# Optimization experiments

Measured on AMD Instinct MI355X. Metric: run time of the kernel, lower is better.

The kernel has to match this reference:

```python
import jax, jax.numpy as jnp
import numpy as np

K = 20
BN_EPS = 1e-5
NEG_SLOPE = 0.2


def knn_idx(x, k):
    # x: [B, C, N]; returns indices of k nearest neighbors per point: [B, N, k]
    sq = jnp.sum(x * x, axis=1)                      # [B, N]
    inner = jnp.einsum('bcn,bcm->bnm', x, x)         # [B, N, N]
    dist = sq[:, :, None] + sq[:, None, :] - 2.0 * inner  # squared distances
    _, idx = jax.lax.top_k(-dist, k)                 # smallest distances
    return idx


def get_graph_feature(x, k):
    # x: [B, C, N] -> [B, 2C, N, k]
    idx = knn_idx(x, k)                               # [B, N, k]
    gather = lambda xb, ib: xb[:, ib]                 # [C,N] x [N,k] -> [C,N,k]
    feature = jax.vmap(gather)(x, idx)                # [B, C, N, k]
    xk = jnp.broadcast_to(x[:, :, :, None], feature.shape)
    return jnp.concatenate([feature - xk, xk], axis=1)  # [B, 2C, N, k]


def setup_inputs() -> dict:
    key = jax.random.key(0)
    k1, k2 = jax.random.split(key)
    B, C, N = 8, 64, 4096
    x = jax.random.normal(k1, (B, C, N), dtype=jnp.float32)
    W = jax.random.normal(k2, (64, 2 * C), dtype=jnp.float32) * (1.0 / np.sqrt(2 * C))
    gamma = jnp.ones((64,), dtype=jnp.float32)
    beta = jnp.zeros((64,), dtype=jnp.float32)
    return {"x": x, "W": W, "gamma": gamma, "beta": beta}


def reference(x, W, gamma, beta):
    g = get_graph_feature(x, K)                       # [B, 2C, N, k]
    y = jnp.einsum('oc,bcnk->bonk', W, g)             # 1x1 conv, no bias
    # BatchNorm2d (training-mode batch statistics) over (B, N, k) per channel
    mean = jnp.mean(y, axis=(0, 2, 3), keepdims=True)
    var = jnp.var(y, axis=(0, 2, 3), keepdims=True)
    y = (y - mean) * jax.lax.rsqrt(var + BN_EPS)
    y = y * gamma[None, :, None, None] + beta[None, :, None, None]
    # LeakyReLU(0.2)
    y = jnp.where(y >= 0, y, NEG_SLOPE * y)
    # max over neighbors
    return jnp.max(y, axis=-1)                        # [B, out, N]
```

## Files before the change

### kernel.cpp

```cpp
#include <hip/hip_runtime.h>
#include <hip/hip_bf16.h>
#include <float.h>

#define BATCH 8
#define CDIM 64
#define NPTS 4096
#define KNN 20
#define KSEL 32
#define BUFCAP 128
#define BN_EPS 1e-5f
#define NEG_SLOPE 0.2f

typedef __attribute__((ext_vector_type(8))) short short8;
typedef __attribute__((ext_vector_type(4))) float float4v;
typedef unsigned short ushort;
typedef unsigned int uint;
typedef unsigned long long ull;

__device__ __forceinline__ ushort f2bf(float f) {
    uint u = __float_as_uint(f);
    u += 0x7FFF + ((u >> 16) & 1);
    return (ushort)(u >> 16);
}
__device__ __forceinline__ int mbcnt64(ull m) {
    int c = __builtin_amdgcn_mbcnt_lo((uint)m, 0);
    return __builtin_amdgcn_mbcnt_hi((uint)(m >> 32), c);
}

__device__ __forceinline__ uint select33_truncate(uint* __restrict__ buf,
                                                  int& cnt, int lane) {
    uint e0 = 0xFFFFFFFFu, e1 = 0xFFFFFFFFu;
    if (lane < cnt) e0 = buf[lane];
    if (64 + lane < cnt) e1 = buf[64 + lane];
    uint p = 0;
    for (int bit = 31; bit >= 0; --bit) {
        uint t = p | (1u << bit);
        ull mA = __ballot(e0 < t);
        ull mB = __ballot(e1 < t);
        if (__popcll(mA) + __popcll(mB) < 33) p = t;
    }
    ull mA = __ballot(e0 < p);
    ull mB = __ballot(e1 < p);
    int pA = __popcll(mA);
    int r0 = mbcnt64(mA);
    int r1 = pA + mbcnt64(mB);
    if (e0 < p) buf[r0] = e0;
    if (e1 < p) buf[r1] = e1;
    cnt = pA + __popcll(mB);
    return p;
}

__device__ __forceinline__ void scan_append(float dwv, float base, int idx,
                                            uint& tau, int& cnt,
                                            uint* __restrict__ buf, int lane) {
    float dval = fmaxf(fmaf(-2.f, dwv, base), 0.f);
    uint key = (__float_as_uint(dval) & 0xFFFFF000u) | (uint)idx;
    ull mask = __ballot(key < tau);
    if (mask) {
        int c = __popcll(mask);
        if (cnt + c > BUFCAP) {
            tau = select33_truncate(buf, cnt, lane);
            mask = __ballot(key < tau);
            c = __popcll(mask);
        }
        if (c) {
            int rank = mbcnt64(mask);
            if (key < tau) buf[cnt + rank] = key;
            cnt += c;
        }
    }
}

__global__ void __launch_bounds__(256) k_ppz(
        const float* __restrict__ x, const float* __restrict__ W,
        float* __restrict__ xt, ushort* __restrict__ xh,
        float* __restrict__ sq,
        float* __restrict__ pt, float* __restrict__ zt) {
    __shared__ float xs[64][65];
    __shared__ float sqred[4][64];

    int b  = blockIdx.x >> 6;
    int n0 = (blockIdx.x & 63) << 6;
    int lane = threadIdx.x & 63;
    int w = threadIdx.x >> 6;
    int row = b * NPTS + n0 + lane;

    const float* xb = x + (size_t)b * CDIM * NPTS + (n0 + lane);
    float v[16]; ushort h[16];
    float accq = 0.f;
    #pragma unroll
    for (int j = 0; j < 16; ++j) {
        float tv = xb[((w << 4) + j) * NPTS];
        v[j] = tv;
        accq = fmaf(tv, tv, accq);
        h[j] = f2bf(tv);
        xs[lane][(w << 4) + j] = tv;
    }
    {
        float4* xtv = (float4*)(xt + ((size_t)row << 6) + (w << 4));
        #pragma unroll
        for (int q = 0; q < 4; ++q)
            xtv[q] = make_float4(v[q*4], v[q*4+1], v[q*4+2], v[q*4+3]);
        uint4* xhp = (uint4*)(xh + ((size_t)row << 6) + (w << 4));
        uint4 p0, p1;
        p0.x = (uint)h[0] | ((uint)h[1] << 16);
        p0.y = (uint)h[2] | ((uint)h[3] << 16);
        p0.z = (uint)h[4] | ((uint)h[5] << 16);
        p0.w = (uint)h[6] | ((uint)h[7] << 16);
        p1.x = (uint)h[8] | ((uint)h[9] << 16);
        p1.y = (uint)h[10] | ((uint)h[11] << 16);
        p1.z = (uint)h[12] | ((uint)h[13] << 16);
        p1.w = (uint)h[14] | ((uint)h[15] << 16);
        xhp[0] = p0; xhp[1] = p1;
    }
    sqred[w][lane] = accq;
    __syncthreads();
    if (w == 0)
        sq[row] = sqred[0][lane] + sqred[1][lane] +
                  sqred[2][lane] + sqred[3][lane];

    size_t rowoff = ((size_t)row) << 6;
    float acc1[16], acc2[16];
    #pragma unroll
    for (int i = 0; i < 16; ++i) { acc1[i] = 0.f; acc2[i] = 0.f; }
    #pragma unroll
    for (int cg = 0; cg < 4; ++cg) {
        float xv[16];
        #pragma unroll
        for (int j = 0; j < 16; ++j)
            xv[j] = xs[lane][(cg << 4) + j];
        #pragma unroll
        for (int oi = 0; oi < 16; ++oi) {
            int o = (w << 4) + oi;
            const float* wr = W + o * 128 + cg * 16;
            float a1 = acc1[oi], a2 = acc2[oi];
            #pragma unroll
            for (int j = 0; j < 16; ++j) {
                a1 = fmaf(wr[j],      xv[j], a1);
                a2 = fmaf(wr[64 + j], xv[j], a2);
            }
            acc1[oi] = a1; acc2[oi] = a2;
        }
    }
    float4* pv = (float4*)(pt + rowoff + (w << 4));
    float4* zv = (float4*)(zt + rowoff + (w << 4));
    #pragma unroll
    for (int q = 0; q < 4; ++q) {
        pv[q] = make_float4(acc1[q*4], acc1[q*4+1], acc1[q*4+2], acc1[q*4+3]);
        zv[q] = make_float4(acc2[q*4]   - acc1[q*4],
                            acc2[q*4+1] - acc1[q*4+1],
                            acc2[q*4+2] - acc1[q*4+2],
                            acc2[q*4+3] - acc1[q*4+3]);
    }
}

__global__ void __launch_bounds__(256, 8) k_knn(
        const ushort* __restrict__ xh,
        const float* __restrict__ sq, ushort* __restrict__ knn32) {
    __shared__ float dw[2][64][20];
    __shared__ uint rowbuf[16 * BUFCAP];

    int tid  = threadIdx.x;
    int t    = tid >> 6;
    int lane = tid & 63;
    int b    = blockIdx.x >> 8;
    int r0   = (blockIdx.x & 255) << 4;
    int col  = lane & 15;
    int quad = lane >> 4;

    size_t arow = ((size_t)(b * NPTS + r0 + col)) << 6;
    short8 ah0 = *(const short8*)(xh + arow + quad * 8);
    short8 ah1 = *(const short8*)(xh + arow + 32 + quad * 8);

    const ushort* xhb = xh + (((size_t)b * NPTS) << 6);
    const float* sqb = sq + b * NPTS;
    const ushort* fbase = xhb + (((size_t)((t << 4) + col)) << 6) + (quad << 3);

    uint tau[4];
    int cnt[4];
    float sqr[4];
    uint* wbuf = rowbuf + ((t << 2) * BUFCAP);
    #pragma unroll
    for (int r = 0; r < 4; ++r) {
        tau[r] = 0xFFFFFFFFu; cnt[r] = 0;
        sqr[r] = sqb[r0 + (t << 2) + r];
    }

    short8 fA0 = *(const short8*)fbase;
    short8 fA1 = *(const short8*)(fbase + 32);
    short8 fB0, fB1;
    float sv_cur = 0.f;
    float sv_nxt = sqb[lane];

    auto step = [&](int c, int q, short8& f0, short8& f1,
                    short8& nf0, short8& nf1) {
        if (c + 1 < 64) {
            const ushort* p = fbase + (((size_t)(c + 1)) << 12);
            nf0 = *(const short8*)p;
            nf1 = *(const short8*)(p + 32);
        }
        float sv_tmp = (c + 1 < 64) ? sqb[((c + 1) << 6) + lane] : 0.f;

        float4v acc = {0.f, 0.f, 0.f, 0.f};
        acc = __builtin_amdgcn_mfma_f32_16x16x32_bf16(ah0, f0, acc, 0, 0, 0);
        acc = __builtin_amdgcn_mfma_f32_16x16x32_bf16(ah1, f1, acc, 0, 0, 0);
        *(float4v*)&dw[q][(t << 4) + col][quad << 2] = acc;

        if (c > 0) {
            int m0 = (c - 1) << 6;
            float4v dv4 = *(const float4v*)&dw[q ^ 1][lane][t << 2];
            #pragma unroll
            for (int r = 0; r < 4; ++r) {
                scan_append(dv4[r], sv_cur + sqr[r], m0 + lane, tau[r], cnt[r],
                            wbuf + r * BUFCAP, lane);
            }
        }
        sv_cur = sv_nxt;
        sv_nxt = sv_tmp;

        __builtin_amdgcn_sched_barrier(0);
        asm volatile("s_waitcnt lgkmcnt(0)" ::: "memory");
        __builtin_amdgcn_s_barrier();
        __builtin_amdgcn_sched_barrier(0);
    };

    for (int c = 0; c < 64; c += 2) {
        step(c,     0, fA0, fA1, fB0, fB1);
        step(c + 1, 1, fB0, fB1, fA0, fA1);
    }

    {
        int m0 = 63 << 6;
        float4v dv4 = *(const float4v*)&dw[1][lane][t << 2];
        #pragma unroll
        for (int r = 0; r < 4; ++r) {
            scan_append(dv4[r], sv_cur + sqr[r], m0 + lane, tau[r], cnt[r],
                        wbuf + r * BUFCAP, lane);
        }
    }

    #pragma unroll
    for (int r = 0; r < 4; ++r) {
        select33_truncate(wbuf + r * BUFCAP, cnt[r], lane);
        if (lane < KSEL) {
            uint e = wbuf[r * BUFCAP + lane];
            knn32[(size_t)(b * NPTS + r0 + (t << 2) + r) * KSEL + lane] =
                (ushort)(e & 0xFFFu);
        }
    }
}

__global__ void __launch_bounds__(256) k_refine(
        const float* __restrict__ xt, const float* __restrict__ sq,
        const ushort* __restrict__ knn32, int* __restrict__ idx20) {
    int wvid = (blockIdx.x << 2) + (threadIdx.x >> 6);
    int lane = threadIdx.x & 63;
    int half = lane >> 5;
    int sl   = lane & 31;
    int row  = (wvid << 1) + half;
    int b = row >> 12;
    int cand = knn32[(size_t)row * KSEL + sl];
    const float4* xc = (const float4*)(xt + ((size_t)(b * NPTS + cand) << 6));
    const float4* xr = (const float4*)(xt + ((size_t)row << 6));
    float acc = 0.f;
    #pragma unroll
    for (int q = 0; q < 16; ++q) {
        float4 a = xr[q], c = xc[q];
        acc = fmaf(a.x, c.x, acc); acc = fmaf(a.y, c.y, acc);
        acc = fmaf(a.z, c.z, acc); acc = fmaf(a.w, c.w, acc);
    }
    float d = fmaf(-2.f, acc, sq[b * NPTS + cand]);
    int rank = 0;
    int base = half << 5;
    #pragma unroll
    for (int j = 0; j < KSEL; ++j) {
        float dj = __shfl(d, base + j);
        int   cj = __shfl(cand, base + j);
        rank += ((dj < d) || (dj == d && cj < cand)) ? 1 : 0;
    }
    if (rank < KNN)
        idx20[(size_t)row * KNN + rank] = cand;
}

__global__ void k_gather(const float* __restrict__ pt, const float* __restrict__ zt,
                         const int* __restrict__ idxin,
                         float* __restrict__ tmax, float* __restrict__ tmin,
                         float* __restrict__ S1, float* __restrict__ S2) {
    __shared__ float red1[4][64];
    __shared__ float red2[4][64];
    int b  = blockIdx.x >> 6;
    int n0 = (blockIdx.x & 63) << 6;
    int lane = threadIdx.x & 63;
    int w = threadIdx.x >> 6;
    float cs1 = 0.f, cs2 = 0.f;
    for (int i = 0; i < 16; ++i) {
        int n = n0 + (w << 4) + i;
        int base = b * NPTS + n;
        int ibase = __builtin_amdgcn_readfirstlane(base * KNN);
        const int* ip = idxin + ibase;
        float mx = -FLT_MAX, mn = FLT_MAX, s1 = 0.f, s2 = 0.f;
        #pragma unroll
        for (int k = 0; k < KNN; ++k) {
            int colp = ip[k];
            float v = pt[(((size_t)(b * NPTS + colp)) << 6) + lane];
            mx = fmaxf(mx, v); mn = fminf(mn, v);
            s1 += v; s2 = fmaf(v, v, s2);
        }
        float z = zt[(((size_t)base) << 6) + lane];
        tmax[(((size_t)base) << 6) + lane] = mx + z;
        tmin[(((size_t)base) << 6) + lane] = mn + z;
        cs1 += s1 + (float)KNN * z;
        cs2 += s2 + 2.f * z * s1 + (float)KNN * z * z;
    }
    red1[w][lane] = cs1;
    red2[w][lane] = cs2;
    __syncthreads();
    if (threadIdx.x < 64) {
        float t1 = red1[0][lane] + red1[1][lane] + red1[2][lane] + red1[3][lane];
        float t2 = red2[0][lane] + red2[1][lane] + red2[2][lane] + red2[3][lane];
        atomicAdd(&S1[lane], t1);
        atomicAdd(&S2[lane], t2);
    }
}

__global__ void k_final(const float* __restrict__ tmax, const float* __restrict__ tmin,
                        const float* __restrict__ S1, const float* __restrict__ S2,
                        const float* __restrict__ gamma, const float* __restrict__ beta,
                        float* __restrict__ out) {
    __shared__ float smx[64][65];
    __shared__ float smn[64][65];
    int b  = blockIdx.x >> 6;
    int n0 = (blockIdx.x & 63) << 6;
    int lane = threadIdx.x & 63;
    int w = threadIdx.x >> 6;
    #pragma unroll
    for (int i = 0; i < 16; ++i) {
        int nl = (i << 2) + w;
        size_t off = (((size_t)(b * NPTS + n0 + nl)) << 6) + lane;
        smx[nl][lane] = tmax[off];
        smn[nl][lane] = tmin[off];
    }
    __syncthreads();
    const float inv_cnt = 1.0f / ((float)BATCH * NPTS * KNN);
    #pragma unroll
    for (int i = 0; i < 16; ++i) {
        int o = (i << 2) + w;
        float s1 = S1[o], s2 = S2[o];
        float mean = s1 * inv_cnt;
        float var = fmaf(-mean, mean, s2 * inv_cnt);
        float rs = rsqrtf(var + BN_EPS);
        float sc = gamma[o] * rs;
        float sh = beta[o] - mean * sc;
        float tv = (sc >= 0.f) ? smx[lane][o] : smn[lane][o];
        float y = fmaf(tv, sc, sh);
        y = (y >= 0.f) ? y : NEG_SLOPE * y;
        out[((size_t)(b * 64 + o)) * NPTS + n0 + lane] = y;
    }
}

extern "C" void kernel_launch(void* const* d_in, const int* in_sizes, int n_in,
                              void* d_out, int out_size, void* d_ws, size_t ws_size,
                              hipStream_t stream) {
    const float* x     = (const float*)d_in[0];
    const float* W     = (const float*)d_in[1];
    const float* gamma = (const float*)d_in[2];
    const float* beta  = (const float*)d_in[3];
    float* out = (float*)d_out;

    float* ws = (float*)d_ws;
    const size_t SECT = (size_t)BATCH * NPTS * 64;
    float*  xt    = ws;
    float*  pt    = ws + SECT;
    float*  zt    = ws + 2 * SECT;
    float*  sq    = ws + 3 * SECT;
    float*  S1    = ws + 3 * SECT + 32768;
    float*  S2    = S1 + 64;
    int*    idx20 = (int*)(ws + 3 * SECT + 32768 + 128);
    float*  uA    = ws + 3 * SECT + 32768 + 128 + 655360;
    ushort* xh    = (ushort*)uA;
    ushort* knn32 = (ushort*)(uA + SECT / 2);
    float*  tmx   = uA;
    float*  tmn   = uA + SECT;

    hipMemsetAsync(S1, 0, 2 * 64 * sizeof(float), stream);
    k_ppz   <<<dim3(BATCH * (NPTS / 64)), dim3(256), 0, stream>>>(x, W, xt, xh, sq, pt, zt);
    k_knn   <<<dim3(BATCH * (NPTS / 16)), dim3(256), 0, stream>>>(xh, sq, knn32);
    k_refine<<<dim3((BATCH * NPTS) / 8), dim3(256), 0, stream>>>(xt, sq, knn32, idx20);
    k_gather<<<dim3(BATCH * (NPTS / 64)), dim3(256), 0, stream>>>(pt, zt, idx20, tmx, tmn, S1, S2);
    k_final <<<dim3(BATCH * (NPTS / 64)), dim3(256), 0, stream>>>(tmx, tmn, S1, S2, gamma, beta, out);
}
```

Before: 328.4 us.

## Fuse kNN refinement into kNN kernel and merge gather/final via grid barrier

The exact-distance refinement of the 32 bf16 candidates now runs inside k_knn, reading them straight from shared memory instead of round-tripping through a global knn32 buffer and a separate launch. The gather and final BN/LeakyReLU kernels are merged: per-point max/min stay in LDS, and an atomic-counter grid barrier waits for the global BN statistics before the output is written. This removes two launches and the tmax/tmin global traffic. The barrier assumes all 512 blocks are co-resident, which risks deadlock if occupancy drops, and the extra refinement work in k_knn may lower that kernel's occupancy.

After: 357.5 us. 8.8% more time.

```diff
diff --git a/kernel.cpp b/kernel.cpp
--- a/kernel.cpp
+++ b/kernel.cpp
@@ -155,8 +155,8 @@
 }
 
 __global__ void __launch_bounds__(256, 8) k_knn(
-        const ushort* __restrict__ xh,
-        const float* __restrict__ sq, ushort* __restrict__ knn32) {
+        const ushort* __restrict__ xh, const float* __restrict__ xt,
+        const float* __restrict__ sq, int* __restrict__ idx20) {
     __shared__ float dw[2][64][20];
     __shared__ uint rowbuf[16 * BUFCAP];
 
@@ -240,62 +240,58 @@
     }
 
     #pragma unroll
-    for (int r = 0; r < 4; ++r) {
+    for (int r = 0; r < 4; ++r)
         select33_truncate(wbuf + r * BUFCAP, cnt[r], lane);
-        if (lane < KSEL) {
-            uint e = wbuf[r * BUFCAP + lane];
-            knn32[(size_t)(b * NPTS + r0 + (t << 2) + r) * KSEL + lane] =
-                (ushort)(e & 0xFFFu);
-        }
-    }
-}
-
-__global__ void __launch_bounds__(256) k_refine(
-        const float* __restrict__ xt, const float* __restrict__ sq,
-        const ushort* __restrict__ knn32, int* __restrict__ idx20) {
-    int wvid = (blockIdx.x << 2) + (threadIdx.x >> 6);
-    int lane = threadIdx.x & 63;
-    int half = lane >> 5;
-    int sl   = lane & 31;
-    int row  = (wvid << 1) + half;
-    int b = row >> 12;
-    int cand = knn32[(size_t)row * KSEL + sl];
-    const float4* xc = (const float4*)(xt + ((size_t)(b * NPTS + cand) << 6));
-    const float4* xr = (const float4*)(xt + ((size_t)row << 6));
-    float acc = 0.f;
-    #pragma unroll
-    for (int q = 0; q < 16; ++q) {
-        float4 a = xr[q], c = xc[q];
-        acc = fmaf(a.x, c.x, acc); acc = fmaf(a.y, c.y, acc);
-        acc = fmaf(a.z, c.z, acc); acc = fmaf(a.w, c.w, acc);
-    }
-    float d = fmaf(-2.f, acc, sq[b * NPTS + cand]);
-    int rank = 0;
-    int base = half << 5;
-    #pragma unroll
-    for (int j = 0; j < KSEL; ++j) {
-        float dj = __shfl(d, base + j);
-        int   cj = __shfl(cand, base + j);
-        rank += ((dj < d) || (dj == d && cj < cand)) ? 1 : 0;
-    }
-    if (rank < KNN)
-        idx20[(size_t)row * KNN + rank] = cand;
-}
-
-__global__ void k_gather(const float* __restrict__ pt, const float* __restrict__ zt,
-                         const int* __restrict__ idxin,
-                         float* __restrict__ tmax, float* __restrict__ tmin,
-                         float* __restrict__ S1, float* __restrict__ S2) {
+
+    #pragma unroll 1
+    for (int pr = 0; pr < 2; ++pr) {
+        int rloc = (pr << 1) + (lane >> 5);
+        int sl   = lane & 31;
+        int cand = (int)(wbuf[rloc * BUFCAP + sl] & 0xFFFu);
+        int grow = r0 + (t << 2) + rloc;
+        const float4* xc = (const float4*)(xt + ((size_t)(b * NPTS + cand) << 6));
+        const float4* xr = (const float4*)(xt + ((size_t)(b * NPTS + grow) << 6));
+        float acc = 0.f;
+        #pragma unroll
+        for (int q = 0; q < 16; ++q) {
+            float4 a = xr[q], c4 = xc[q];
+            acc = fmaf(a.x, c4.x, acc); acc = fmaf(a.y, c4.y, acc);
+            acc = fmaf(a.z, c4.z, acc); acc = fmaf(a.w, c4.w, acc);
+        }
+        float d = fmaf(-2.f, acc, sqb[cand]);
+        int rank = 0;
+        int base = (lane >> 5) << 5;
+        #pragma unroll
+        for (int j = 0; j < KSEL; ++j) {
+            float dj = __shfl(d, base + j);
+            int   cj = __shfl(cand, base + j);
+            rank += ((dj < d) || (dj == d && cj < cand)) ? 1 : 0;
+        }
+        if (rank < KNN)
+            idx20[(size_t)(b * NPTS + grow) * KNN + rank] = cand;
+    }
+}
+
+__global__ void __launch_bounds__(256) k_gf(
+        const float* __restrict__ pt, const float* __restrict__ zt,
+        const int* __restrict__ idxin,
+        const float* __restrict__ gamma, const float* __restrict__ beta,
+        float* __restrict__ S1, float* __restrict__ S2,
+        int* __restrict__ counter, float* __restrict__ out) {
+    __shared__ float smax[64][65];
+    __shared__ float smin[64][65];
     __shared__ float red1[4][64];
     __shared__ float red2[4][64];
+
     int b  = blockIdx.x >> 6;
     int n0 = (blockIdx.x & 63) << 6;
     int lane = threadIdx.x & 63;
     int w = threadIdx.x >> 6;
+
     float cs1 = 0.f, cs2 = 0.f;
     for (int i = 0; i < 16; ++i) {
-        int n = n0 + (w << 4) + i;
-        int base = b * NPTS + n;
+        int nl = (w << 4) + i;
+        int base = b * NPTS + n0 + nl;
         int ibase = __builtin_amdgcn_readfirstlane(base * KNN);
         const int* ip = idxin + ibase;
         float mx = -FLT_MAX, mn = FLT_MAX, s1 = 0.f, s2 = 0.f;
@@ -307,8 +303,8 @@
             s1 += v; s2 = fmaf(v, v, s2);
         }
         float z = zt[(((size_t)base) << 6) + lane];
-        tmax[(((size_t)base) << 6) + lane] = mx + z;
-        tmin[(((size_t)base) << 6) + lane] = mn + z;
+        smax[nl][lane] = mx + z;
+        smin[nl][lane] = mn + z;
         cs1 += s1 + (float)KNN * z;
         cs2 += s2 + 2.f * z * s1 + (float)KNN * z * z;
     }
@@ -321,37 +317,31 @@
         atomicAdd(&S1[lane], t1);
         atomicAdd(&S2[lane], t2);
     }
-}
-
-__global__ void k_final(const float* __restrict__ tmax, const float* __restrict__ tmin,
-                        const float* __restrict__ S1, const float* __restrict__ S2,
-                        const float* __restrict__ gamma, const float* __restrict__ beta,
-                        float* __restrict__ out) {
-    __shared__ float smx[64][65];
-    __shared__ float smn[64][65];
-    int b  = blockIdx.x >> 6;
-    int n0 = (blockIdx.x & 63) << 6;
-    int lane = threadIdx.x & 63;
-    int w = threadIdx.x >> 6;
-    #pragma unroll
-    for (int i = 0; i < 16; ++i) {
-        int nl = (i << 2) + w;
-        size_t off = (((size_t)(b * NPTS + n0 + nl)) << 6) + lane;
-        smx[nl][lane] = tmax[off];
-        smn[nl][lane] = tmin[off];
-    }
     __syncthreads();
+
+    if (threadIdx.x == 0) {
+        __hip_atomic_fetch_add(counter, 1, __ATOMIC_ACQ_REL,
+                               __HIP_MEMORY_SCOPE_AGENT);
+        while (__hip_atomic_load(counter, __ATOMIC_ACQUIRE,
+                                 __HIP_MEMORY_SCOPE_AGENT) < (int)gridDim.x)
+            __builtin_amdgcn_s_sleep(8);
+    }
+    __syncthreads();
+
     const float inv_cnt = 1.0f / ((float)BATCH * NPTS * KNN);
     #pragma unroll
     for (int i = 0; i < 16; ++i) {
         int o = (i << 2) + w;
-        float s1 = S1[o], s2 = S2[o];
+        float s1 = __hip_atomic_load(&S1[o], __ATOMIC_RELAXED,
+                                     __HIP_MEMORY_SCOPE_AGENT);
+        float s2 = __hip_atomic_load(&S2[o], __ATOMIC_RELAXED,
+                                     __HIP_MEMORY_SCOPE_AGENT);
         float mean = s1 * inv_cnt;
         float var = fmaf(-mean, mean, s2 * inv_cnt);
         float rs = rsqrtf(var + BN_EPS);
         float sc = gamma[o] * rs;
         float sh = beta[o] - mean * sc;
-        float tv = (sc >= 0.f) ? smx[lane][o] : smn[lane][o];
+        float tv = (sc >= 0.f) ? smax[lane][o] : smin[lane][o];
         float y = fmaf(tv, sc, sh);
         y = (y >= 0.f) ? y : NEG_SLOPE * y;
         out[((size_t)(b * 64 + o)) * NPTS + n0 + lane] = y;
@@ -375,17 +365,12 @@
     float*  sq    = ws + 3 * SECT;
     float*  S1    = ws + 3 * SECT + 32768;
     float*  S2    = S1 + 64;
-    int*    idx20 = (int*)(ws + 3 * SECT + 32768 + 128);
-    float*  uA    = ws + 3 * SECT + 32768 + 128 + 655360;
-    ushort* xh    = (ushort*)uA;
-    ushort* knn32 = (ushort*)(uA + SECT / 2);
-    float*  tmx   = uA;
-    float*  tmn   = uA + SECT;
-
-    hipMemsetAsync(S1, 0, 2 * 64 * sizeof(float), stream);
-    k_ppz   <<<dim3(BATCH * (NPTS / 64)), dim3(256), 0, stream>>>(x, W, xt, xh, sq, pt, zt);
-    k_knn   <<<dim3(BATCH * (NPTS / 16)), dim3(256), 0, stream>>>(xh, sq, knn32);
-    k_refine<<<dim3((BATCH * NPTS) / 8), dim3(256), 0, stream>>>(xt, sq, knn32, idx20);
-    k_gather<<<dim3(BATCH * (NPTS / 64)), dim3(256), 0, stream>>>(pt, zt, idx20, tmx, tmn, S1, S2);
-    k_final <<<dim3(BATCH * (NPTS / 64)), dim3(256), 0, stream>>>(tmx, tmn, S1, S2, gamma, beta, out);
-}
+    int*    cnt   = (int*)(S1 + 128);
+    int*    idx20 = (int*)(S1 + 160);
+    ushort* xh    = (ushort*)(S1 + 160 + 655360);
+
+    hipMemsetAsync(S1, 0, 160 * sizeof(float), stream);
+    k_ppz <<<dim3(BATCH * (NPTS / 64)), dim3(256), 0, stream>>>(x, W, xt, xh, sq, pt, zt);
+    k_knn <<<dim3(BATCH * (NPTS / 16)), dim3(256), 0, stream>>>(xh, xt, sq, idx20);
+    k_gf  <<<dim3(BATCH * (NPTS / 64)), dim3(256), 0, stream>>>(pt, zt, idx20, gamma, beta, S1, S2, cnt, out);
+}
```

## Recompute neighbor max/min in final kernel instead of storing intermediates

Applied to the files above, without the earlier changes.

The gather kernel now only accumulates BatchNorm sums and no longer writes per-point max and min tensors. The final kernel re-gathers neighbor features through the kNN indices, picks max or min per channel from the sign of the BN scale, and applies BN and LeakyReLU directly. This removes the write and read-back of two large intermediate buffers, at the cost of a second pass of gathered reads that relies on cache hits.

New measurement: 337.1 us. 1.03x slower.

```diff
diff --git a/kernel.cpp b/kernel.cpp
--- a/kernel.cpp
+++ b/kernel.cpp
@@ -282,10 +282,9 @@
         idx20[(size_t)row * KNN + rank] = cand;
 }
 
-__global__ void k_gather(const float* __restrict__ pt, const float* __restrict__ zt,
-                         const int* __restrict__ idxin,
-                         float* __restrict__ tmax, float* __restrict__ tmin,
-                         float* __restrict__ S1, float* __restrict__ S2) {
+__global__ void k_stat(const float* __restrict__ pt, const float* __restrict__ zt,
+                       const int* __restrict__ idxin,
+                       float* __restrict__ S1, float* __restrict__ S2) {
     __shared__ float red1[4][64];
     __shared__ float red2[4][64];
     int b  = blockIdx.x >> 6;
@@ -298,17 +297,14 @@
         int base = b * NPTS + n;
         int ibase = __builtin_amdgcn_readfirstlane(base * KNN);
         const int* ip = idxin + ibase;
-        float mx = -FLT_MAX, mn = FLT_MAX, s1 = 0.f, s2 = 0.f;
+        float s1 = 0.f, s2 = 0.f;
         #pragma unroll
         for (int k = 0; k < KNN; ++k) {
             int colp = ip[k];
             float v = pt[(((size_t)(b * NPTS + colp)) << 6) + lane];
-            mx = fmaxf(mx, v); mn = fminf(mn, v);
             s1 += v; s2 = fmaf(v, v, s2);
         }
         float z = zt[(((size_t)base) << 6) + lane];
-        tmax[(((size_t)base) << 6) + lane] = mx + z;
-        tmin[(((size_t)base) << 6) + lane] = mn + z;
         cs1 += s1 + (float)KNN * z;
         cs2 += s2 + 2.f * z * s1 + (float)KNN * z * z;
     }
@@ -323,38 +319,50 @@
     }
 }
 
-__global__ void k_final(const float* __restrict__ tmax, const float* __restrict__ tmin,
-                        const float* __restrict__ S1, const float* __restrict__ S2,
-                        const float* __restrict__ gamma, const float* __restrict__ beta,
-                        float* __restrict__ out) {
-    __shared__ float smx[64][65];
-    __shared__ float smn[64][65];
+__global__ void __launch_bounds__(256) k_fin(
+        const float* __restrict__ pt, const float* __restrict__ zt,
+        const int* __restrict__ idxin,
+        const float* __restrict__ S1, const float* __restrict__ S2,
+        const float* __restrict__ gamma, const float* __restrict__ beta,
+        float* __restrict__ out) {
+    __shared__ float sy[64][65];
     int b  = blockIdx.x >> 6;
     int n0 = (blockIdx.x & 63) << 6;
     int lane = threadIdx.x & 63;
     int w = threadIdx.x >> 6;
-    #pragma unroll
+
+    const float inv_cnt = 1.0f / ((float)BATCH * NPTS * KNN);
+    float s1 = S1[lane], s2 = S2[lane];
+    float mean = s1 * inv_cnt;
+    float var = fmaf(-mean, mean, s2 * inv_cnt);
+    float rs = rsqrtf(var + BN_EPS);
+    float sc = gamma[lane] * rs;
+    float sh = beta[lane] - mean * sc;
+    bool useMax = (sc >= 0.f);
+
     for (int i = 0; i < 16; ++i) {
-        int nl = (i << 2) + w;
-        size_t off = (((size_t)(b * NPTS + n0 + nl)) << 6) + lane;
-        smx[nl][lane] = tmax[off];
-        smn[nl][lane] = tmin[off];
+        int nl = (w << 4) + i;
+        int base = b * NPTS + n0 + nl;
+        int ibase = __builtin_amdgcn_readfirstlane(base * KNN);
+        const int* ip = idxin + ibase;
+        float mx = -FLT_MAX, mn = FLT_MAX;
+        #pragma unroll
+        for (int k = 0; k < KNN; ++k) {
+            int colp = ip[k];
+            float v = pt[(((size_t)(b * NPTS + colp)) << 6) + lane];
+            mx = fmaxf(mx, v); mn = fminf(mn, v);
+        }
+        float z = zt[(((size_t)base) << 6) + lane];
+        float tv = (useMax ? mx : mn) + z;
+        float y = fmaf(tv, sc, sh);
+        y = (y >= 0.f) ? y : NEG_SLOPE * y;
+        sy[nl][lane] = y;
     }
     __syncthreads();
-    const float inv_cnt = 1.0f / ((float)BATCH * NPTS * KNN);
     #pragma unroll
     for (int i = 0; i < 16; ++i) {
         int o = (i << 2) + w;
-        float s1 = S1[o], s2 = S2[o];
-        float mean = s1 * inv_cnt;
-        float var = fmaf(-mean, mean, s2 * inv_cnt);
-        float rs = rsqrtf(var + BN_EPS);
-        float sc = gamma[o] * rs;
-        float sh = beta[o] - mean * sc;
-        float tv = (sc >= 0.f) ? smx[lane][o] : smn[lane][o];
-        float y = fmaf(tv, sc, sh);
-        y = (y >= 0.f) ? y : NEG_SLOPE * y;
-        out[((size_t)(b * 64 + o)) * NPTS + n0 + lane] = y;
+        out[((size_t)(b * 64 + o)) * NPTS + n0 + lane] = sy[lane][o];
     }
 }
 
@@ -375,17 +383,15 @@
     float*  sq    = ws + 3 * SECT;
     float*  S1    = ws + 3 * SECT + 32768;
     float*  S2    = S1 + 64;
-    int*    idx20 = (int*)(ws + 3 * SECT + 32768 + 128);
+    int*    idx20 = (int*)(S1 + 128);
     float*  uA    = ws + 3 * SECT + 32768 + 128 + 655360;
     ushort* xh    = (ushort*)uA;
     ushort* knn32 = (ushort*)(uA + SECT / 2);
-    float*  tmx   = uA;
-    float*  tmn   = uA + SECT;
-
-    hipMemsetAsync(S1, 0, 2 * 64 * sizeof(float), stream);
+
+    hipMemsetAsync(S1, 0, 128 * sizeof(float), stream);
     k_ppz   <<<dim3(BATCH * (NPTS / 64)), dim3(256), 0, stream>>>(x, W, xt, xh, sq, pt, zt);
     k_knn   <<<dim3(BATCH * (NPTS / 16)), dim3(256), 0, stream>>>(xh, sq, knn32);
     k_refine<<<dim3((BATCH * NPTS) / 8), dim3(256), 0, stream>>>(xt, sq, knn32, idx20);
-    k_gather<<<dim3(BATCH * (NPTS / 64)), dim3(256), 0, stream>>>(pt, zt, idx20, tmx, tmn, S1, S2);
-    k_final <<<dim3(BATCH * (NPTS / 64)), dim3(256), 0, stream>>>(tmx, tmn, S1, S2, gamma, beta, out);
-}
+    k_stat  <<<dim3(BATCH * (NPTS / 64)), dim3(256), 0, stream>>>(pt, zt, idx20, S1, S2);
+    k_fin   <<<dim3(BATCH * (NPTS / 64)), dim3(256), 0, stream>>>(pt, zt, idx20, S1, S2, gamma, beta, out);
+}
```
